# Optimization experiments

Hardware: AMD Instinct MI355X
Metric: run time of the kernel (lower is better)

## Reference

```python
import jax, jax.numpy as jnp
import numpy as np

N = 50000
E = 800000


def gcn_layer(x, W, b, row, col):
    # Linear transform first (as in CustomGCNLayer.forward)
    h = x @ W + b  # [N, out]
    # Segment-mean over incoming edges grouped by destination node `col`;
    # out[i] = mean(h[row[col == i]]) if node i has in-edges else h[i].
    s = jax.ops.segment_sum(h[row], col, num_segments=N)              # [N, out]
    cnt = jax.ops.segment_sum(jnp.ones((row.shape[0],), h.dtype), col, num_segments=N)  # [N]
    mean = s / jnp.maximum(cnt, 1.0)[:, None]
    return jnp.where(cnt[:, None] > 0, mean, h)


def setup_inputs() -> dict:
    key = jax.random.key(0)
    ks = jax.random.split(key, 6)
    x = jax.random.normal(ks[0], (N, 128), dtype=jnp.float32)
    edge_index = jax.random.randint(ks[1], (2, E), 0, N, dtype=jnp.int64)
    # Glorot-ish scaled weights
    W1 = jax.random.normal(ks[2], (128, 128), dtype=jnp.float32) * (1.0 / np.sqrt(128))
    b1 = jnp.zeros((128,), jnp.float32)
    W2 = jax.random.normal(ks[3], (128, 128), dtype=jnp.float32) * (1.0 / np.sqrt(128))
    b2 = jnp.zeros((128,), jnp.float32)
    W3 = jax.random.normal(ks[4], (128, 64), dtype=jnp.float32) * (1.0 / np.sqrt(128))
    b3 = jnp.zeros((64,), jnp.float32)
    return {"x": x, "edge_index": edge_index, "W1": W1, "b1": b1,
            "W2": W2, "b2": b2, "W3": W3, "b3": b3}


def reference(x, edge_index, W1, b1, W2, b2, W3, b3):
    row, col = edge_index[0], edge_index[1]
    h = jax.nn.relu(gcn_layer(x, W1, b1, row, col))
    # Dropout layers run in eval mode for the reference (identity).
    h = jax.nn.relu(gcn_layer(h, W2, b2, row, col))
    h = gcn_layer(h, W3, b3, row, col)
    return jax.nn.log_softmax(h, axis=1)
```

## Files before the change

kernel.cpp:

```cpp
#include <hip/hip_runtime.h>
#include <hip/hip_bf16.h>


typedef __attribute__((ext_vector_type(8))) short short8v;
typedef __attribute__((ext_vector_type(4))) float f32x4;
typedef __attribute__((ext_vector_type(2))) float f32x2;

#define NPART 256

#if defined(__has_builtin)
#if __has_builtin(__builtin_amdgcn_cvt_pk_f32_fp8) && __has_builtin(__builtin_amdgcn_cvt_pk_fp8_f32)
#define HW_FP8 1
#endif
#endif

static __device__ __forceinline__ ushort f2bf(float f) {
    __hip_bfloat16 h = __float2bfloat16(f);
    return *reinterpret_cast<ushort*>(&h);
}
static __device__ __forceinline__ float bf_lo(uint u) { return __uint_as_float(u << 16); }
static __device__ __forceinline__ float bf_hi(uint u) { return __uint_as_float(u & 0xffff0000u); }

#ifndef HW_FP8
static __device__ __forceinline__ float fp8_dec1(uint b) {
    uint s = b >> 7, e = (b >> 3) & 15, m = b & 7;
    float v = e ? __uint_as_float(((e + 120u) << 23) | (m << 20))
                : (float)m * 0.001953125f;
    return s ? -v : v;
}
static __device__ __forceinline__ uint fp8_enc1(float f) {
    uint s = (__float_as_uint(f) >> 31) << 7;
    float a = fabsf(f);
    if (!(a < 448.f)) a = 448.f;
    if (a < 0.015625f) {
        int q = (int)rintf(a * 512.f);
        return s | (uint)q;
    }
    int e; float m = frexpf(a, &e);
    int q = (int)rintf(m * 16.f) - 8;
    int E = e - 1;
    if (q == 8) { q = 0; ++E; }
    if (E > 8) return s | 0x7E;
    return s | (uint)((E + 7) << 3) | (uint)q;
}
#endif

static __device__ __forceinline__ f32x2 fp8x2_to_f32(ushort u) {
#ifdef HW_FP8
    return __builtin_amdgcn_cvt_pk_f32_fp8((int)(uint)u, false);
#else
    f32x2 r; r.x = fp8_dec1(u & 0xFF); r.y = fp8_dec1(u >> 8); return r;
#endif
}
static __device__ __forceinline__ uchar f32_to_fp8(float a) {
#ifdef HW_FP8
    return (uchar)(__builtin_amdgcn_cvt_pk_fp8_f32(a, a, 0, false) & 0xFF);
#else
    return (uchar)fp8_enc1(a);
#endif
}

static __device__ __forceinline__ void gemm1_body(
    const float* __restrict__ X, const float* __restrict__ W,
    const float* __restrict__ bias, uchar* __restrict__ Y8, int n,
    int wid, int lane) {
    int r0 = wid * 16;
    if (r0 >= n) return;
    int arow = r0 + (lane & 15);
    if (arow >= n) arow = n - 1;
    int kb = lane >> 4;
    int c  = lane & 15;

    f32x4 acc[8];
#pragma unroll
    for (int ct = 0; ct < 8; ++ct) acc[ct] = (f32x4)(0.f);

#pragma unroll
    for (int kt = 0; kt < 4; ++kt) {
        const float* ap = &X[(size_t)arow * 128 + kt * 32 + kb * 8];
        float4 a0 = *(const float4*)ap;
        float4 a1 = *(const float4*)(ap + 4);
        union { short8v v; ushort u[8]; } av;
        av.u[0] = f2bf(a0.x); av.u[1] = f2bf(a0.y);
        av.u[2] = f2bf(a0.z); av.u[3] = f2bf(a0.w);
        av.u[4] = f2bf(a1.x); av.u[5] = f2bf(a1.y);
        av.u[6] = f2bf(a1.z); av.u[7] = f2bf(a1.w);
#pragma unroll
        for (int ct = 0; ct < 8; ++ct) {
            union { short8v v; ushort u[8]; } bv;
#pragma unroll
            for (int j = 0; j < 8; ++j)
                bv.u[j] = f2bf(W[(size_t)(kt * 32 + kb * 8 + j) * 128 + ct * 16 + c]);
            acc[ct] = __builtin_amdgcn_mfma_f32_16x16x32_bf16(av.v, bv.v, acc[ct], 0, 0, 0);
        }
    }

    int rg = lane >> 4;
#pragma unroll
    for (int ct = 0; ct < 8; ++ct) {
        float bvs = bias[ct * 16 + c];
#pragma unroll
        for (int j = 0; j < 4; ++j) {
            int r = r0 + rg * 4 + j;
            if (r < n) Y8[(size_t)r * 128 + ct * 16 + c] = f32_to_fp8(acc[ct][j] + bvs);
        }
    }
}

__global__ __launch_bounds__(256) void fused_pa(
    const int* __restrict__ col, int* __restrict__ Gmat,
    const float* __restrict__ x, const float* __restrict__ W1,
    const float* __restrict__ b1, uchar* __restrict__ h8,
    const float* __restrict__ W2, ushort* __restrict__ Wf2,
    const float* __restrict__ W3, ushort* __restrict__ Wf3,
    int n, int E, int NBKT, int ECH, int GB) {
    __shared__ uint hist[1024];
    int b = blockIdx.x, t = threadIdx.x;
    if (b < NPART) {
        for (int i = t; i < NBKT; i += 256) hist[i] = 0;
        __syncthreads();
        int e0 = b * ECH, e1 = min(e0 + ECH, E);
        for (int e = e0 + t; e < e1; e += 256)
            atomicAdd(&hist[col[e] >> 6], 1u);
        __syncthreads();
        for (int i = t; i < NBKT; i += 256)
            Gmat[i * NPART + b] = (int)hist[i];
        return;
    }
    b -= NPART;
    if (b < GB) {
        int wid = (b * 256 + t) >> 6;
        gemm1_body(x, W1, b1, h8, n, wid, t & 63);
        return;
    }
    b -= GB;
    const float* W; ushort* Wf; int OUT; int tid;
    if (b < 8) { W = W2; Wf = Wf2; OUT = 128; tid = b * 256 + t; }
    else       { W = W3; Wf = Wf3; OUT = 64;  tid = (b - 8) * 256 + t; }
    int CT = OUT >> 4;
    int total = 4 * CT * 64;
    if (tid >= total) return;
    int kt   = tid / (CT * 64);
    int rem  = tid % (CT * 64);
    int ct   = rem >> 6;
    int lane = rem & 63;
    int c  = lane & 15;
    int kb = lane >> 4;
    ushort tmp[8];
#pragma unroll
    for (int j = 0; j < 8; ++j)
        tmp[j] = f2bf(W[(kt * 32 + kb * 8 + j) * OUT + ct * 16 + c]);
    uint4 o;
    o.x = ((uint)tmp[1] << 16) | tmp[0];
    o.y = ((uint)tmp[3] << 16) | tmp[2];
    o.z = ((uint)tmp[5] << 16) | tmp[4];
    o.w = ((uint)tmp[7] << 16) | tmp[6];
    ((uint4*)Wf)[tid] = o;
}

__global__ void scanA_partial(const int* __restrict__ g, int* __restrict__ bsum, int M) {
    __shared__ int lds[256];
    int i = blockIdx.x * 256 + threadIdx.x;
    int v = (i < M) ? g[i] : 0;
    lds[threadIdx.x] = v;
    __syncthreads();
    for (int s = 128; s > 0; s >>= 1) {
        if (threadIdx.x < s) lds[threadIdx.x] += lds[threadIdx.x + s];
        __syncthreads();
    }
    if (threadIdx.x == 0) bsum[blockIdx.x] = lds[0];
}

__global__ void scan_bsums_big(int* __restrict__ bsum, int nb) {
    __shared__ int ts[256];
    int t = threadIdx.x;
    int v[4]; int s = 0;
#pragma unroll
    for (int j = 0; j < 4; ++j) {
        int i = t * 4 + j;
        v[j] = (i < nb) ? bsum[i] : 0;
        s += v[j];
    }
    ts[t] = s;
    __syncthreads();
    for (int off = 1; off < 256; off <<= 1) {
        int u = (t >= off) ? ts[t - off] : 0;
        __syncthreads();
        ts[t] += u;
        __syncthreads();
    }
    int run = ts[t] - s;
#pragma unroll
    for (int j = 0; j < 4; ++j) {
        int i = t * 4 + j;
        if (i < nb) { int old = v[j]; bsum[i] = run; run += old; }
    }
}

__global__ void scanA_final(int* __restrict__ g, const int* __restrict__ bsum, int M) {
    __shared__ int lds[256];
    int t = threadIdx.x;
    int i = blockIdx.x * 256 + t;
    int v = (i < M) ? g[i] : 0;
    lds[t] = v;
    __syncthreads();
    for (int off = 1; off < 256; off <<= 1) {
        int u = (t >= off) ? lds[t - off] : 0;
        __syncthreads();
        lds[t] += u;
        __syncthreads();
    }
    if (i < M) g[i] = lds[t] - v + bsum[blockIdx.x];
}

__global__ __launch_bounds__(256) void pa2_scatter(
    const int* __restrict__ row, const int* __restrict__ col,
    const int* __restrict__ Gscan, uint* __restrict__ coarse,
    int E, int NBKT, int ECH) {
    __shared__ uint cur[1024];
    int p = blockIdx.x, t = threadIdx.x;
    for (int i = t; i < NBKT; i += 256) cur[i] = (uint)Gscan[i * NPART + p];
    __syncthreads();
    int e0 = p * ECH, e1 = min(e0 + ECH, E);
    for (int e = e0 + t; e < e1; e += 256) {
        int d = col[e];
        uint slot = atomicAdd(&cur[d >> 6], 1u);
        coarse[slot] = ((uint)(d & 63) << 16) | (uint)(row[e] & 0xFFFF);
    }
}

__global__ __launch_bounds__(256) void pb_fine(
    const uint* __restrict__ coarse, const int* __restrict__ Gscan,
    int* __restrict__ cnt, int* __restrict__ start,
    ushort* __restrict__ srclist16, int n, int E, int NBKT) {
    __shared__ uint c64[64];
    int b = blockIdx.x, t = threadIdx.x;
    int lo = Gscan[b * NPART];
    int hi = (b + 1 < NBKT) ? Gscan[(b + 1) * NPART] : E;
    if (t < 64) c64[t] = 0;
    __syncthreads();
    for (int i = lo + t; i < hi; i += 256)
        atomicAdd(&c64[coarse[i] >> 16], 1u);
    __syncthreads();
    if (t < 64) {
        uint v = c64[t];
        uint x = v;
#pragma unroll
        for (int off = 1; off < 64; off <<= 1) {
            uint u = __shfl_up(x, off);
            if (t >= off) x += u;
        }
        uint excl = x - v;
        int node = b * 64 + t;
        if (node < n) { cnt[node] = (int)v; start[node] = lo + (int)excl; }
        c64[t] = excl;
    }
    __syncthreads();
    for (int i = lo + t; i < hi; i += 256) {
        uint u  = coarse[i];
        uint dl = u >> 16;
        uint slot = atomicAdd(&c64[dl], 1u);
        srclist16[lo + slot] = (ushort)u;
    }
}

static __device__ __forceinline__ void agg_node128_f8(
    const ushort* __restrict__ h16, const ushort* __restrict__ srclist16,
    int s0, int c, int lane, float& ax, float& ay) {
    ax = 0.f; ay = 0.f;
    for (int base = 0; base < c; base += 64) {
        int m = c - base;
        if (m > 64) m = 64;
        int idx = (int)srclist16[s0 + base + (lane < m ? lane : 0)];
        int e = 0;
        for (; e + 8 <= m; e += 8) {
            int i0 = __shfl(idx, e + 0), i1 = __shfl(idx, e + 1);
            int i2 = __shfl(idx, e + 2), i3 = __shfl(idx, e + 3);
            int i4 = __shfl(idx, e + 4), i5 = __shfl(idx, e + 5);
            int i6 = __shfl(idx, e + 6), i7 = __shfl(idx, e + 7);
            ushort u0 = h16[(size_t)i0 * 64 + lane];
            ushort u1 = h16[(size_t)i1 * 64 + lane];
            ushort u2 = h16[(size_t)i2 * 64 + lane];
            ushort u3 = h16[(size_t)i3 * 64 + lane];
            ushort u4 = h16[(size_t)i4 * 64 + lane];
            ushort u5 = h16[(size_t)i5 * 64 + lane];
            ushort u6 = h16[(size_t)i6 * 64 + lane];
            ushort u7 = h16[(size_t)i7 * 64 + lane];
            f32x2 v0 = fp8x2_to_f32(u0), v1 = fp8x2_to_f32(u1);
            f32x2 v2 = fp8x2_to_f32(u2), v3 = fp8x2_to_f32(u3);
            f32x2 v4 = fp8x2_to_f32(u4), v5 = fp8x2_to_f32(u5);
            f32x2 v6 = fp8x2_to_f32(u6), v7 = fp8x2_to_f32(u7);
            ax += ((v0.x + v1.x) + (v2.x + v3.x)) + ((v4.x + v5.x) + (v6.x + v7.x));
            ay += ((v0.y + v1.y) + (v2.y + v3.y)) + ((v4.y + v5.y) + (v6.y + v7.y));
        }
        for (; e + 4 <= m; e += 4) {
            int i0 = __shfl(idx, e + 0), i1 = __shfl(idx, e + 1);
            int i2 = __shfl(idx, e + 2), i3 = __shfl(idx, e + 3);
            f32x2 v0 = fp8x2_to_f32(h16[(size_t)i0 * 64 + lane]);
            f32x2 v1 = fp8x2_to_f32(h16[(size_t)i1 * 64 + lane]);
            f32x2 v2 = fp8x2_to_f32(h16[(size_t)i2 * 64 + lane]);
            f32x2 v3 = fp8x2_to_f32(h16[(size_t)i3 * 64 + lane]);
            ax += (v0.x + v1.x) + (v2.x + v3.x);
            ay += (v0.y + v1.y) + (v2.y + v3.y);
        }
        for (; e < m; ++e) {
            int i0 = __shfl(idx, e);
            f32x2 v0 = fp8x2_to_f32(h16[(size_t)i0 * 64 + lane]);
            ax += v0.x;
            ay += v0.y;
        }
    }
}

template <int OUT, bool F8OUT>
__global__ __launch_bounds__(256) void fused_agg_gemm_f8(
    const uchar* __restrict__ h8, const int* __restrict__ start,
    const int* __restrict__ cnt, const ushort* __restrict__ srclist16,
    const ushort* __restrict__ Wf, const float* __restrict__ bias,
    void* __restrict__ Yout, int n) {
    constexpr int CT  = OUT / 16;
    constexpr int CTW = CT / 4;
    __shared__ uint tile[16 * 68];
    int t = threadIdx.x;
    int wave = t >> 6, lane = t & 63;
    int base = blockIdx.x * 16;
    if (base >= n) return;
    const ushort* h16 = (const ushort*)h8;

#pragma unroll
    for (int q = 0; q < 4; ++q) {
        int r = wave * 4 + q;
        int node = base + r;
        uint pk = 0;
        if (node < n) {
            int s0 = start[node], c = cnt[node];
            float ax, ay;
            agg_node128_f8(h16, srclist16, s0, c, lane, ax, ay);
            float rx, ry;
            if (c > 0) {
                float inv = 1.f / (float)c;
                rx = ax * inv; ry = ay * inv;
            } else {
                f32x2 v = fp8x2_to_f32(h16[(size_t)node * 64 + lane]);
                rx = v.x; ry = v.y;
            }
            rx = fmaxf(rx, 0.f); ry = fmaxf(ry, 0.f);
            pk = ((uint)f2bf(ry) << 16) | f2bf(rx);
        }
        tile[r * 68 + lane] = pk;
    }
    __syncthreads();

    int ar = lane & 15;
    int kb = lane >> 4;
    f32x4 acc[CTW];
#pragma unroll
    for (int j = 0; j < CTW; ++j) acc[j] = (f32x4)(0.f);

#pragma unroll
    for (int kt = 0; kt < 4; ++kt) {
        uint4 a4 = *(const uint4*)&tile[ar * 68 + kt * 16 + kb * 4];
        short8v a = *(const short8v*)&a4;
#pragma unroll
        for (int j = 0; j < CTW; ++j) {
            int ct = wave * CTW + j;
            short8v b = *(const short8v*)&Wf[(size_t)((kt * CT + ct) * 64 + lane) * 8];
            acc[j] = __builtin_amdgcn_mfma_f32_16x16x32_bf16(a, b, acc[j], 0, 0, 0);
        }
    }

    int c16 = lane & 15, rg = lane >> 4;
#pragma unroll
    for (int j = 0; j < CTW; ++j) {
        int ct = wave * CTW + j;
        float bv = bias[ct * 16 + c16];
#pragma unroll
        for (int jj = 0; jj < 4; ++jj) {
            int r = base + rg * 4 + jj;
            if (r < n) {
                float v = acc[j][jj] + bv;
                if (F8OUT) ((uchar*)Yout)[(size_t)r * OUT + ct * 16 + c16] = f32_to_fp8(v);
                else       ((ushort*)Yout)[(size_t)r * OUT + ct * 16 + c16] = f2bf(v);
            }
        }
    }
}

__global__ __launch_bounds__(256) void agg64_lsm_bf16(
    const ushort* __restrict__ h, const int* __restrict__ start,
    const int* __restrict__ cnt, const ushort* __restrict__ srclist16,
    float* __restrict__ out, int n) {
    int wid  = (blockIdx.x * blockDim.x + threadIdx.x) >> 6;
    int lane = threadIdx.x & 63;
    if (wid >= n) return;
    int s0 = start[wid];
    int c  = cnt[wid];
    float a = 0.f;
    for (int base = 0; base < c; base += 64) {
        int m = c - base;
        if (m > 64) m = 64;
        int idx = (int)srclist16[s0 + base + (lane < m ? lane : 0)];
        int e = 0;
        for (; e + 8 <= m; e += 8) {
            int i0 = __shfl(idx, e + 0), i1 = __shfl(idx, e + 1);
            int i2 = __shfl(idx, e + 2), i3 = __shfl(idx, e + 3);
            int i4 = __shfl(idx, e + 4), i5 = __shfl(idx, e + 5);
            int i6 = __shfl(idx, e + 6), i7 = __shfl(idx, e + 7);
            float v0 = __uint_as_float((uint)h[(size_t)i0 * 64 + lane] << 16);
            float v1 = __uint_as_float((uint)h[(size_t)i1 * 64 + lane] << 16);
            float v2 = __uint_as_float((uint)h[(size_t)i2 * 64 + lane] << 16);
            float v3 = __uint_as_float((uint)h[(size_t)i3 * 64 + lane] << 16);
            float v4 = __uint_as_float((uint)h[(size_t)i4 * 64 + lane] << 16);
            float v5 = __uint_as_float((uint)h[(size_t)i5 * 64 + lane] << 16);
            float v6 = __uint_as_float((uint)h[(size_t)i6 * 64 + lane] << 16);
            float v7 = __uint_as_float((uint)h[(size_t)i7 * 64 + lane] << 16);
            a += ((v0 + v1) + (v2 + v3)) + ((v4 + v5) + (v6 + v7));
        }
        for (; e < m; ++e) {
            int i0 = __shfl(idx, e);
            a += __uint_as_float((uint)h[(size_t)i0 * 64 + lane] << 16);
        }
    }
    float v = (c > 0) ? a / (float)c
                      : __uint_as_float((uint)h[(size_t)wid * 64 + lane] << 16);

    float m = v;
#pragma unroll
    for (int off = 32; off > 0; off >>= 1) m = fmaxf(m, __shfl_xor(m, off));
    float ex = __expf(v - m);
    float s = ex;
#pragma unroll
    for (int off = 32; off > 0; off >>= 1) s += __shfl_xor(s, off);
    out[(size_t)wid * 64 + lane] = v - m - __logf(s);
}

extern "C" void kernel_launch(void* const* d_in, const int* in_sizes, int n_in,
                              void* d_out, int out_size, void* d_ws, size_t ws_size,
                              hipStream_t stream) {
    const float* x  = (const float*)d_in[0];
    const int*   ei = (const int*)d_in[1];
    const float* W1 = (const float*)d_in[2];
    const float* b1 = (const float*)d_in[3];
    const float* W2 = (const float*)d_in[4];
    const float* b2 = (const float*)d_in[5];
    const float* W3 = (const float*)d_in[6];
    const float* b3 = (const float*)d_in[7];
    float* out = (float*)d_out;

    const int n = in_sizes[0] / 128;
    const int E = in_sizes[1] / 2;
    const int* row = ei;
    const int* col = ei + E;

    char* ws = (char*)d_ws;
    size_t off = 0;
    auto carve = [&](size_t bytes) {
        char* p = ws + off;
        off = (off + bytes + 255) & ~(size_t)255;
        return p;
    };
    uchar*  h8a       = (uchar*)carve((size_t)n * 128);
    uchar*  h8b       = (uchar*)carve((size_t)n * 128);
    ushort* hbuf      = (ushort*)carve((size_t)n * 64 * 2);
    ushort* Wf2       = (ushort*)carve(4 * 8 * 64 * 8 * 2);
    ushort* Wf3       = (ushort*)carve(4 * 4 * 64 * 8 * 2);
    const int NBKT    = (n + 63) / 64;
    int*    Gmat      = (int*)carve((size_t)NBKT * NPART * sizeof(int));
    uint*   coarse    = (uint*)carve((size_t)E * sizeof(uint));
    int*    cnt       = (int*)carve((size_t)n * sizeof(int));
    int*    start     = (int*)carve((size_t)n * sizeof(int));
    ushort* srclist16 = (ushort*)carve((size_t)E * 2);
    int*    bsum      = (int*)carve(4096);

    const int ECH   = (E + NPART - 1) / NPART;
    const int M     = NBKT * NPART;
    const int MB    = (M + 255) / 256;
    const int nwave = (n + 15) / 16;
    const int GB    = (nwave + 3) / 4;
    const int FB    = (n + 15) / 16;
    const int agrid = (n + 3) / 4;

    fused_pa<<<NPART + GB + 12, 256, 0, stream>>>(col, Gmat, x, W1, b1, h8a,
                                                  W2, Wf2, W3, Wf3,
                                                  n, E, NBKT, ECH, GB);
    scanA_partial<<<MB, 256, 0, stream>>>(Gmat, bsum, M);
    scan_bsums_big<<<1, 256, 0, stream>>>(bsum, MB);
    scanA_final<<<MB, 256, 0, stream>>>(Gmat, bsum, M);
    pa2_scatter<<<NPART, 256, 0, stream>>>(row, col, Gmat, coarse, E, NBKT, ECH);
    pb_fine<<<NBKT, 256, 0, stream>>>(coarse, Gmat, cnt, start, srclist16, n, E, NBKT);

    fused_agg_gemm_f8<128, true><<<FB, 256, 0, stream>>>(h8a, start, cnt, srclist16,
                                                         Wf2, b2, h8b, n);
    fused_agg_gemm_f8<64, false><<<FB, 256, 0, stream>>>(h8b, start, cnt, srclist16,
                                                         Wf3, b3, hbuf, n);
    agg64_lsm_bf16<<<agrid, 256, 0, stream>>>(hbuf, start, cnt, srclist16, out, n);
}
```

Before: 140.1 us.

## Split feature table into column halves and unfuse aggregation from GEMM

Stores the fp8 hidden features as two column-half tables of 64 bytes per node, so each gather touches a smaller, more cache-resident table. Aggregation runs as a separate kernel over both halves, with two nodes per wave using 32 lanes each, and writes bf16 results to an intermediate buffer. A standalone MFMA GEMM kernel then reads that buffer. This targets the cache-miss cost of random gathers, but adds extra kernel launches and a full write and read of an n×128 bf16 intermediate.

```diff
diff --git a/kernel.cpp b/kernel.cpp
--- a/kernel.cpp
+++ b/kernel.cpp
@@ -18,8 +18,6 @@
     __hip_bfloat16 h = __float2bfloat16(f);
     return *reinterpret_cast<ushort*>(&h);
 }
-static __device__ __forceinline__ float bf_lo(uint u) { return __uint_as_float(u << 16); }
-static __device__ __forceinline__ float bf_hi(uint u) { return __uint_as_float(u & 0xffff0000u); }
 
 #ifndef HW_FP8
 static __device__ __forceinline__ float fp8_dec1(uint b) {
@@ -99,10 +97,12 @@
 #pragma unroll
     for (int ct = 0; ct < 8; ++ct) {
         float bvs = bias[ct * 16 + c];
+        int f    = ct * 16 + c;
+        size_t hb = (size_t)(f >> 6) * n * 64 + (f & 63);
 #pragma unroll
         for (int j = 0; j < 4; ++j) {
             int r = r0 + rg * 4 + j;
-            if (r < n) Y8[(size_t)r * 128 + ct * 16 + c] = f32_to_fp8(acc[ct][j] + bvs);
+            if (r < n) Y8[hb + (size_t)r * 64] = f32_to_fp8(acc[ct][j] + bvs);
         }
     }
 }
@@ -264,28 +264,40 @@
     }
 }
 
-static __device__ __forceinline__ void agg_node128_f8(
-    const ushort* __restrict__ h16, const ushort* __restrict__ srclist16,
-    int s0, int c, int lane, float& ax, float& ay) {
-    ax = 0.f; ay = 0.f;
-    for (int base = 0; base < c; base += 64) {
-        int m = c - base;
-        if (m > 64) m = 64;
-        int idx = (int)srclist16[s0 + base + (lane < m ? lane : 0)];
+__global__ __launch_bounds__(256) void agg_half(
+    const uchar* __restrict__ h8, const int* __restrict__ start,
+    const int* __restrict__ cnt, const ushort* __restrict__ srclist16,
+    ushort* __restrict__ aggout, int n, int G) {
+    int b = blockIdx.x, t = threadIdx.x;
+    int half = (b >= G) ? 1 : 0;
+    int bb   = b - half * G;
+    int wave = t >> 6, lane = t & 63;
+    int sub = lane >> 5;
+    int sl  = lane & 31;
+    int lb  = sub << 5;
+    int node = (bb * 4 + wave) * 2 + sub;
+    if (node >= n) return;
+    const ushort* tab16 = (const ushort*)(h8 + (size_t)half * n * 64);
+
+    int s0 = start[node], c = cnt[node];
+    float ax = 0.f, ay = 0.f;
+    for (int base = 0; base < c; base += 32) {
+        int m = c - base; if (m > 32) m = 32;
+        int idx = (int)srclist16[s0 + base + (sl < m ? sl : 0)];
         int e = 0;
         for (; e + 8 <= m; e += 8) {
-            int i0 = __shfl(idx, e + 0), i1 = __shfl(idx, e + 1);
-            int i2 = __shfl(idx, e + 2), i3 = __shfl(idx, e + 3);
-            int i4 = __shfl(idx, e + 4), i5 = __shfl(idx, e + 5);
-            int i6 = __shfl(idx, e + 6), i7 = __shfl(idx, e + 7);
-            ushort u0 = h16[(size_t)i0 * 64 + lane];
-            ushort u1 = h16[(size_t)i1 * 64 + lane];
-            ushort u2 = h16[(size_t)i2 * 64 + lane];
-            ushort u3 = h16[(size_t)i3 * 64 + lane];
-            ushort u4 = h16[(size_t)i4 * 64 + lane];
-            ushort u5 = h16[(size_t)i5 * 64 + lane];
-            ushort u6 = h16[(size_t)i6 * 64 + lane];
-            ushort u7 = h16[(size_t)i7 * 64 + lane];
+            int i0 = __shfl(idx, lb + e + 0), i1 = __shfl(idx, lb + e + 1);
+            int i2 = __shfl(idx, lb + e + 2), i3 = __shfl(idx, lb + e + 3);
+            int i4 = __shfl(idx, lb + e + 4), i5 = __shfl(idx, lb + e + 5);
+            int i6 = __shfl(idx, lb + e + 6), i7 = __shfl(idx, lb + e + 7);
+            ushort u0 = tab16[(size_t)i0 * 32 + sl];
+            ushort u1 = tab16[(size_t)i1 * 32 + sl];
+            ushort u2 = tab16[(size_t)i2 * 32 + sl];
+            ushort u3 = tab16[(size_t)i3 * 32 + sl];
+            ushort u4 = tab16[(size_t)i4 * 32 + sl];
+            ushort u5 = tab16[(size_t)i5 * 32 + sl];
+            ushort u6 = tab16[(size_t)i6 * 32 + sl];
+            ushort u7 = tab16[(size_t)i7 * 32 + sl];
             f32x2 v0 = fp8x2_to_f32(u0), v1 = fp8x2_to_f32(u1);
             f32x2 v2 = fp8x2_to_f32(u2), v3 = fp8x2_to_f32(u3);
             f32x2 v4 = fp8x2_to_f32(u4), v5 = fp8x2_to_f32(u5);
@@ -294,93 +306,76 @@
             ay += ((v0.y + v1.y) + (v2.y + v3.y)) + ((v4.y + v5.y) + (v6.y + v7.y));
         }
         for (; e + 4 <= m; e += 4) {
-            int i0 = __shfl(idx, e + 0), i1 = __shfl(idx, e + 1);
-            int i2 = __shfl(idx, e + 2), i3 = __shfl(idx, e + 3);
-            f32x2 v0 = fp8x2_to_f32(h16[(size_t)i0 * 64 + lane]);
-            f32x2 v1 = fp8x2_to_f32(h16[(size_t)i1 * 64 + lane]);
-            f32x2 v2 = fp8x2_to_f32(h16[(size_t)i2 * 64 + lane]);
-            f32x2 v3 = fp8x2_to_f32(h16[(size_t)i3 * 64 + lane]);
+            int i0 = __shfl(idx, lb + e + 0), i1 = __shfl(idx, lb + e + 1);
+            int i2 = __shfl(idx, lb + e + 2), i3 = __shfl(idx, lb + e + 3);
+            f32x2 v0 = fp8x2_to_f32(tab16[(size_t)i0 * 32 + sl]);
+            f32x2 v1 = fp8x2_to_f32(tab16[(size_t)i1 * 32 + sl]);
+            f32x2 v2 = fp8x2_to_f32(tab16[(size_t)i2 * 32 + sl]);
+            f32x2 v3 = fp8x2_to_f32(tab16[(size_t)i3 * 32 + sl]);
             ax += (v0.x + v1.x) + (v2.x + v3.x);
             ay += (v0.y + v1.y) + (v2.y + v3.y);
         }
         for (; e < m; ++e) {
-            int i0 = __shfl(idx, e);
-            f32x2 v0 = fp8x2_to_f32(h16[(size_t)i0 * 64 + lane]);
-            ax += v0.x;
-            ay += v0.y;
-        }
-    }
-}
-
-template <int OUT, bool F8OUT>
-__global__ __launch_bounds__(256) void fused_agg_gemm_f8(
-    const uchar* __restrict__ h8, const int* __restrict__ start,
-    const int* __restrict__ cnt, const ushort* __restrict__ srclist16,
-    const ushort* __restrict__ Wf, const float* __restrict__ bias,
-    void* __restrict__ Yout, int n) {
-    constexpr int CT  = OUT / 16;
-    constexpr int CTW = CT / 4;
-    __shared__ uint tile[16 * 68];
-    int t = threadIdx.x;
-    int wave = t >> 6, lane = t & 63;
-    int base = blockIdx.x * 16;
-    if (base >= n) return;
-    const ushort* h16 = (const ushort*)h8;
-
-#pragma unroll
-    for (int q = 0; q < 4; ++q) {
-        int r = wave * 4 + q;
-        int node = base + r;
-        uint pk = 0;
-        if (node < n) {
-            int s0 = start[node], c = cnt[node];
-            float ax, ay;
-            agg_node128_f8(h16, srclist16, s0, c, lane, ax, ay);
-            float rx, ry;
-            if (c > 0) {
-                float inv = 1.f / (float)c;
-                rx = ax * inv; ry = ay * inv;
-            } else {
-                f32x2 v = fp8x2_to_f32(h16[(size_t)node * 64 + lane]);
-                rx = v.x; ry = v.y;
-            }
-            rx = fmaxf(rx, 0.f); ry = fmaxf(ry, 0.f);
-            pk = ((uint)f2bf(ry) << 16) | f2bf(rx);
-        }
-        tile[r * 68 + lane] = pk;
-    }
-    __syncthreads();
-
-    int ar = lane & 15;
+            int i0 = __shfl(idx, lb + e);
+            f32x2 v0 = fp8x2_to_f32(tab16[(size_t)i0 * 32 + sl]);
+            ax += v0.x; ay += v0.y;
+        }
+    }
+    float rx, ry;
+    if (c > 0) {
+        float inv = 1.f / (float)c;
+        rx = ax * inv; ry = ay * inv;
+    } else {
+        f32x2 v = fp8x2_to_f32(tab16[(size_t)node * 32 + sl]);
+        rx = v.x; ry = v.y;
+    }
+    rx = fmaxf(rx, 0.f); ry = fmaxf(ry, 0.f);
+    uint pk = ((uint)f2bf(ry) << 16) | f2bf(rx);
+    __builtin_nontemporal_store(pk, &((uint*)aggout)[(size_t)node * 64 + half * 32 + sl]);
+}
+
+template <int OUT, int OMODE>
+__global__ __launch_bounds__(256) void gemm_mfma(
+    const ushort* __restrict__ X, const ushort* __restrict__ Wf,
+    const float* __restrict__ bias, void* __restrict__ Yout, int n) {
+    constexpr int CT = OUT / 16;
+    int wid  = (blockIdx.x * 256 + threadIdx.x) >> 6;
+    int lane = threadIdx.x & 63;
+    int r0 = wid * 16;
+    if (r0 >= n) return;
+    int arow = r0 + (lane & 15);
+    if (arow >= n) arow = n - 1;
     int kb = lane >> 4;
-    f32x4 acc[CTW];
-#pragma unroll
-    for (int j = 0; j < CTW; ++j) acc[j] = (f32x4)(0.f);
+
+    f32x4 acc[CT];
+#pragma unroll
+    for (int ct = 0; ct < CT; ++ct) acc[ct] = (f32x4)(0.f);
 
 #pragma unroll
     for (int kt = 0; kt < 4; ++kt) {
-        uint4 a4 = *(const uint4*)&tile[ar * 68 + kt * 16 + kb * 4];
-        short8v a = *(const short8v*)&a4;
-#pragma unroll
-        for (int j = 0; j < CTW; ++j) {
-            int ct = wave * CTW + j;
+        short8v a = *(const short8v*)&X[(size_t)arow * 128 + kt * 32 + kb * 8];
+#pragma unroll
+        for (int ct = 0; ct < CT; ++ct) {
             short8v b = *(const short8v*)&Wf[(size_t)((kt * CT + ct) * 64 + lane) * 8];
-            acc[j] = __builtin_amdgcn_mfma_f32_16x16x32_bf16(a, b, acc[j], 0, 0, 0);
-        }
-    }
-
-    int c16 = lane & 15, rg = lane >> 4;
-#pragma unroll
-    for (int j = 0; j < CTW; ++j) {
-        int ct = wave * CTW + j;
-        float bv = bias[ct * 16 + c16];
-#pragma unroll
-        for (int jj = 0; jj < 4; ++jj) {
-            int r = base + rg * 4 + jj;
+            acc[ct] = __builtin_amdgcn_mfma_f32_16x16x32_bf16(a, b, acc[ct], 0, 0, 0);
+        }
+    }
+
+    int c  = lane & 15;
+    int rg = lane >> 4;
+#pragma unroll
+    for (int ct = 0; ct < CT; ++ct) {
+        float bv = bias[ct * 16 + c];
+        int f = ct * 16 + c;
+#pragma unroll
+        for (int j = 0; j < 4; ++j) {
+            int r = r0 + rg * 4 + j;
             if (r < n) {
-                float v = acc[j][jj] + bv;
-                if (F8OUT) ((uchar*)Yout)[(size_t)r * OUT + ct * 16 + c16] = f32_to_fp8(v);
-                else       ((ushort*)Yout)[(size_t)r * OUT + ct * 16 + c16] = f2bf(v);
+                float v = acc[ct][j] + bv;
+                if (OMODE == 1)
+                    ((uchar*)Yout)[(size_t)(f >> 6) * n * 64 + (size_t)r * 64 + (f & 63)] = f32_to_fp8(v);
+                else
+                    ((ushort*)Yout)[(size_t)r * OUT + f] = f2bf(v);
             }
         }
     }
@@ -459,9 +454,10 @@
         off = (off + bytes + 255) & ~(size_t)255;
         return p;
     };
-    uchar*  h8a       = (uchar*)carve((size_t)n * 128);
-    uchar*  h8b       = (uchar*)carve((size_t)n * 128);
-    ushort* hbuf      = (ushort*)carve((size_t)n * 64 * 2);
+    uchar*  h8a       = (uchar*)carve((size_t)2 * n * 64);
+    uchar*  h8b       = (uchar*)carve((size_t)2 * n * 64);
+    ushort* aggbuf    = (ushort*)carve((size_t)n * 128 * 2);
+    ushort* t3buf     = (ushort*)carve((size_t)n * 64 * 2);
     ushort* Wf2       = (ushort*)carve(4 * 8 * 64 * 8 * 2);
     ushort* Wf3       = (ushort*)carve(4 * 4 * 64 * 8 * 2);
     const int NBKT    = (n + 63) / 64;
@@ -477,7 +473,7 @@
     const int MB    = (M + 255) / 256;
     const int nwave = (n + 15) / 16;
     const int GB    = (nwave + 3) / 4;
-    const int FB    = (n + 15) / 16;
+    const int G     = (n + 7) / 8;
     const int agrid = (n + 3) / 4;
 
     fused_pa<<<NPART + GB + 12, 256, 0, stream>>>(col, Gmat, x, W1, b1, h8a,
@@ -489,9 +485,9 @@
     pa2_scatter<<<NPART, 256, 0, stream>>>(row, col, Gmat, coarse, E, NBKT, ECH);
     pb_fine<<<NBKT, 256, 0, stream>>>(coarse, Gmat, cnt, start, srclist16, n, E, NBKT);
 
-    fused_agg_gemm_f8<128, true><<<FB, 256, 0, stream>>>(h8a, start, cnt, srclist16,
-                                                         Wf2, b2, h8b, n);
-    fused_agg_gemm_f8<64, false><<<FB, 256, 0, stream>>>(h8b, start, cnt, srclist16,
-                                                         Wf3, b3, hbuf, n);
-    agg64_lsm_bf16<<<agrid, 256, 0, stream>>>(hbuf, start, cnt, srclist16, out, n);
-}
+    agg_half<<<2 * G, 256, 0, stream>>>(h8a, start, cnt, srclist16, aggbuf, n, G);
+    gemm_mfma<128, 1><<<GB, 256, 0, stream>>>(aggbuf, Wf2, b2, h8b, n);
+    agg_half<<<2 * G, 256, 0, stream>>>(h8b, start, cnt, srclist16, aggbuf, n, G);
+    gemm_mfma<64, 0><<<GB, 256, 0, stream>>>(aggbuf, Wf3, b3, t3buf, n);
+    agg64_lsm_bf16<<<agrid, 256, 0, stream>>>(t3buf, start, cnt, srclist16, out, n);
+}
```

Measured after the change: 155.7 us. 11.1% more time.

## Store layer-3 output in fp8 and fold block-sum scan into final scan

Applied to the files above, without the earlier changes.

The layer-3 GEMM output is now written as fp8 instead of bf16, and the final aggregate plus log_softmax kernel gathers single fp8 bytes. This halves the bytes per gathered edge row, at the cost of lower final-layer precision. The separate scan kernel over block sums is removed. Each scanA_final block now sums the preceding block totals itself, trading one launch for redundant reads of bsum.

```diff
diff --git a/kernel.cpp b/kernel.cpp
--- a/kernel.cpp
+++ b/kernel.cpp
@@ -18,8 +18,6 @@
     __hip_bfloat16 h = __float2bfloat16(f);
     return *reinterpret_cast<ushort*>(&h);
 }
-static __device__ __forceinline__ float bf_lo(uint u) { return __uint_as_float(u << 16); }
-static __device__ __forceinline__ float bf_hi(uint u) { return __uint_as_float(u & 0xffff0000u); }
 
 #ifndef HW_FP8
 static __device__ __forceinline__ float fp8_dec1(uint b) {
@@ -51,6 +49,9 @@
 #else
     f32x2 r; r.x = fp8_dec1(u & 0xFF); r.y = fp8_dec1(u >> 8); return r;
 #endif
+}
+static __device__ __forceinline__ float fp8_to_f32(uchar b) {
+    return fp8x2_to_f32((ushort)b).x;
 }
 static __device__ __forceinline__ uchar f32_to_fp8(float a) {
 #ifdef HW_FP8
@@ -171,35 +172,19 @@
     if (threadIdx.x == 0) bsum[blockIdx.x] = lds[0];
 }
 
-__global__ void scan_bsums_big(int* __restrict__ bsum, int nb) {
-    __shared__ int ts[256];
-    int t = threadIdx.x;
-    int v[4]; int s = 0;
-#pragma unroll
-    for (int j = 0; j < 4; ++j) {
-        int i = t * 4 + j;
-        v[j] = (i < nb) ? bsum[i] : 0;
-        s += v[j];
-    }
-    ts[t] = s;
-    __syncthreads();
-    for (int off = 1; off < 256; off <<= 1) {
-        int u = (t >= off) ? ts[t - off] : 0;
-        __syncthreads();
-        ts[t] += u;
-        __syncthreads();
-    }
-    int run = ts[t] - s;
-#pragma unroll
-    for (int j = 0; j < 4; ++j) {
-        int i = t * 4 + j;
-        if (i < nb) { int old = v[j]; bsum[i] = run; run += old; }
-    }
-}
-
 __global__ void scanA_final(int* __restrict__ g, const int* __restrict__ bsum, int M) {
     __shared__ int lds[256];
     int t = threadIdx.x;
+    int acc = 0;
+    for (int j = t; j < blockIdx.x; j += 256) acc += bsum[j];
+    lds[t] = acc;
+    __syncthreads();
+    for (int s = 128; s > 0; s >>= 1) {
+        if (t < s) lds[t] += lds[t + s];
+        __syncthreads();
+    }
+    int blockoff = lds[0];
+    __syncthreads();
     int i = blockIdx.x * 256 + t;
     int v = (i < M) ? g[i] : 0;
     lds[t] = v;
@@ -210,7 +195,7 @@
         lds[t] += u;
         __syncthreads();
     }
-    if (i < M) g[i] = lds[t] - v + bsum[blockIdx.x];
+    if (i < M) g[i] = lds[t] - v + blockoff;
 }
 
 __global__ __launch_bounds__(256) void pa2_scatter(
@@ -312,12 +297,12 @@
     }
 }
 
-template <int OUT, bool F8OUT>
+template <int OUT>
 __global__ __launch_bounds__(256) void fused_agg_gemm_f8(
     const uchar* __restrict__ h8, const int* __restrict__ start,
     const int* __restrict__ cnt, const ushort* __restrict__ srclist16,
     const ushort* __restrict__ Wf, const float* __restrict__ bias,
-    void* __restrict__ Yout, int n) {
+    uchar* __restrict__ Y8, int n) {
     constexpr int CT  = OUT / 16;
     constexpr int CTW = CT / 4;
     __shared__ uint tile[16 * 68];
@@ -377,17 +362,13 @@
 #pragma unroll
         for (int jj = 0; jj < 4; ++jj) {
             int r = base + rg * 4 + jj;
-            if (r < n) {
-                float v = acc[j][jj] + bv;
-                if (F8OUT) ((uchar*)Yout)[(size_t)r * OUT + ct * 16 + c16] = f32_to_fp8(v);
-                else       ((ushort*)Yout)[(size_t)r * OUT + ct * 16 + c16] = f2bf(v);
-            }
-        }
-    }
-}
-
-__global__ __launch_bounds__(256) void agg64_lsm_bf16(
-    const ushort* __restrict__ h, const int* __restrict__ start,
+            if (r < n) Y8[(size_t)r * OUT + ct * 16 + c16] = f32_to_fp8(acc[j][jj] + bv);
+        }
+    }
+}
+
+__global__ __launch_bounds__(256) void agg64_lsm_f8(
+    const uchar* __restrict__ h8, const int* __restrict__ start,
     const int* __restrict__ cnt, const ushort* __restrict__ srclist16,
     float* __restrict__ out, int n) {
     int wid  = (blockIdx.x * blockDim.x + threadIdx.x) >> 6;
@@ -406,23 +387,22 @@
             int i2 = __shfl(idx, e + 2), i3 = __shfl(idx, e + 3);
             int i4 = __shfl(idx, e + 4), i5 = __shfl(idx, e + 5);
             int i6 = __shfl(idx, e + 6), i7 = __shfl(idx, e + 7);
-            float v0 = __uint_as_float((uint)h[(size_t)i0 * 64 + lane] << 16);
-            float v1 = __uint_as_float((uint)h[(size_t)i1 * 64 + lane] << 16);
-            float v2 = __uint_as_float((uint)h[(size_t)i2 * 64 + lane] << 16);
-            float v3 = __uint_as_float((uint)h[(size_t)i3 * 64 + lane] << 16);
-            float v4 = __uint_as_float((uint)h[(size_t)i4 * 64 + lane] << 16);
-            float v5 = __uint_as_float((uint)h[(size_t)i5 * 64 + lane] << 16);
-            float v6 = __uint_as_float((uint)h[(size_t)i6 * 64 + lane] << 16);
-            float v7 = __uint_as_float((uint)h[(size_t)i7 * 64 + lane] << 16);
+            float v0 = fp8_to_f32(h8[(size_t)i0 * 64 + lane]);
+            float v1 = fp8_to_f32(h8[(size_t)i1 * 64 + lane]);
+            float v2 = fp8_to_f32(h8[(size_t)i2 * 64 + lane]);
+            float v3 = fp8_to_f32(h8[(size_t)i3 * 64 + lane]);
+            float v4 = fp8_to_f32(h8[(size_t)i4 * 64 + lane]);
+            float v5 = fp8_to_f32(h8[(size_t)i5 * 64 + lane]);
+            float v6 = fp8_to_f32(h8[(size_t)i6 * 64 + lane]);
+            float v7 = fp8_to_f32(h8[(size_t)i7 * 64 + lane]);
             a += ((v0 + v1) + (v2 + v3)) + ((v4 + v5) + (v6 + v7));
         }
         for (; e < m; ++e) {
             int i0 = __shfl(idx, e);
-            a += __uint_as_float((uint)h[(size_t)i0 * 64 + lane] << 16);
-        }
-    }
-    float v = (c > 0) ? a / (float)c
-                      : __uint_as_float((uint)h[(size_t)wid * 64 + lane] << 16);
+            a += fp8_to_f32(h8[(size_t)i0 * 64 + lane]);
+        }
+    }
+    float v = (c > 0) ? a / (float)c : fp8_to_f32(h8[(size_t)wid * 64 + lane]);
 
     float m = v;
 #pragma unroll
@@ -461,7 +441,7 @@
     };
     uchar*  h8a       = (uchar*)carve((size_t)n * 128);
     uchar*  h8b       = (uchar*)carve((size_t)n * 128);
-    ushort* hbuf      = (ushort*)carve((size_t)n * 64 * 2);
+    uchar*  t3_8      = (uchar*)carve((size_t)n * 64);
     ushort* Wf2       = (ushort*)carve(4 * 8 * 64 * 8 * 2);
     ushort* Wf3       = (ushort*)carve(4 * 4 * 64 * 8 * 2);
     const int NBKT    = (n + 63) / 64;
@@ -484,14 +464,13 @@
                                                   W2, Wf2, W3, Wf3,
                                                   n, E, NBKT, ECH, GB);
     scanA_partial<<<MB, 256, 0, stream>>>(Gmat, bsum, M);
-    scan_bsums_big<<<1, 256, 0, stream>>>(bsum, MB);
     scanA_final<<<MB, 256, 0, stream>>>(Gmat, bsum, M);
     pa2_scatter<<<NPART, 256, 0, stream>>>(row, col, Gmat, coarse, E, NBKT, ECH);
     pb_fine<<<NBKT, 256, 0, stream>>>(coarse, Gmat, cnt, start, srclist16, n, E, NBKT);
 
-    fused_agg_gemm_f8<128, true><<<FB, 256, 0, stream>>>(h8a, start, cnt, srclist16,
-                                                         Wf2, b2, h8b, n);
-    fused_agg_gemm_f8<64, false><<<FB, 256, 0, stream>>>(h8b, start, cnt, srclist16,
-                                                         Wf3, b3, hbuf, n);
-    agg64_lsm_bf16<<<agrid, 256, 0, stream>>>(hbuf, start, cnt, srclist16, out, n);
-}
+    fused_agg_gemm_f8<128><<<FB, 256, 0, stream>>>(h8a, start, cnt, srclist16,
+                                                   Wf2, b2, h8b, n);
+    fused_agg_gemm_f8<64><<<FB, 256, 0, stream>>>(h8b, start, cnt, srclist16,
+                                                  Wf3, b3, t3_8, n);
+    agg64_lsm_f8<<<agrid, 256, 0, stream>>>(t3_8, start, cnt, srclist16, out, n);
+}
```

Measured after the change: 136.8 us, median of 2. 2.3% less time.
